# Performance work log

Measured on AMD Instinct MI355X. Metric: run time of the kernel, lower is better.

The kernel has to match this reference:

```python
import jax, jax.numpy as jnp
import numpy as np

N = 100_000      # nodes
E = 1_600_000    # edges (avg degree 16)
F_IN = 128       # dataset.num_features
H = 128          # hidden
C = 25_000       # num_clusters (~ target_ratio 0.25 * N)
G = 64           # graphs in batch
NCLS = 10        # dataset.num_classes


def _gcn_conv(x, w, b, src, dst, n):
    # PyG GCNConv: add self loops, symmetric normalization deg^-1/2 A_hat deg^-1/2
    h = x @ w  # [n, out]
    deg = jnp.zeros((n,), x.dtype).at[dst].add(1.0) + 1.0  # +1 self loop
    dis = jax.lax.rsqrt(deg)
    norm = dis[src] * dis[dst]  # [E]
    out = jnp.zeros_like(h).at[dst].add(h[src] * norm[:, None])
    out = out + h * (dis * dis)[:, None]  # self-loop term norm_ii = deg_i^-1
    return out + b


def _mean_pool(x, seg, num_seg):
    s = jax.ops.segment_sum(x, seg, num_segments=num_seg)
    cnt = jax.ops.segment_sum(jnp.ones((x.shape[0],), x.dtype), seg, num_segments=num_seg)
    return s / jnp.maximum(cnt, 1.0)[:, None]


def _max_pool(x, seg, num_seg):
    m = jax.ops.segment_max(x, seg, num_segments=num_seg)
    cnt = jax.ops.segment_sum(jnp.ones((x.shape[0],), x.dtype), seg, num_segments=num_seg)
    return jnp.where(cnt[:, None] > 0, m, 0.0)


def setup_inputs() -> dict:
    key = jax.random.key(0)
    ks = jax.random.split(key, 12)
    def glorot(k, shape):
        fan_in = shape[0]
        return (jax.random.normal(k, shape, jnp.float32) / np.sqrt(fan_in)).astype(jnp.float32)
    return {
        "x": jax.random.normal(ks[0], (N, F_IN), jnp.float32),
        "edge_index": jax.random.randint(ks[1], (2, E), 0, N, dtype=jnp.int32).astype(jnp.int64),
        "batch": jnp.sort(jax.random.randint(ks[2], (N,), 0, G, dtype=jnp.int32)).astype(jnp.int64),
        "cluster": jax.random.randint(ks[3], (N,), 0, C, dtype=jnp.int32).astype(jnp.int64),
        "num_clusters": C,
        "num_graphs": G,
        "W1": glorot(ks[4], (F_IN, H)), "b1": jnp.zeros((H,), jnp.float32),
        "W2": glorot(ks[5], (H, H)),   "b2": jnp.zeros((H,), jnp.float32),
        "W3": glorot(ks[6], (H, H)),   "b3": jnp.zeros((H,), jnp.float32),
        "lin1_w": glorot(ks[7], (4 * H, H)), "lin1_b": jnp.zeros((H,), jnp.float32),
        "lin2_w": glorot(ks[8], (H, NCLS)),  "lin2_b": jnp.zeros((NCLS,), jnp.float32),
    }


def reference(x, edge_index, batch, cluster, num_clusters, num_graphs,
              W1, b1, W2, b2, W3, b3, lin1_w, lin1_b, lin2_w, lin2_b):
    n = x.shape[0]
    src, dst = edge_index[0], edge_index[1]
    # conv1 + relu (dropout is identity in eval mode)
    h = jax.nn.relu(_gcn_conv(x, W1, b1, src, dst, n))
    pre_mean = _mean_pool(h, batch, num_graphs)
    pre_max = _max_pool(h, batch, num_graphs)
    # LaCorePooling(aggregate='mean'): segment-mean nodes by cluster id,
    # relabel edges to cluster ids, derive pooled batch vector.
    hp = _mean_pool(h, cluster, num_clusters)            # [C, H]
    src_p, dst_p = cluster[src], cluster[dst]            # pooled edge list
    batch_p = jax.ops.segment_max(batch, cluster, num_segments=num_clusters)
    batch_p = jnp.maximum(batch_p, 0)                    # empty clusters -> graph 0
    # post-pool GCN layers
    hp = jax.nn.relu(_gcn_conv(hp, W2, b2, src_p, dst_p, num_clusters))
    hp = jax.nn.relu(_gcn_conv(hp, W3, b3, src_p, dst_p, num_clusters))
    post_mean = _mean_pool(hp, batch_p, num_graphs)
    post_max = _max_pool(hp, batch_p, num_graphs)
    z = jnp.concatenate([pre_mean, pre_max, post_mean, post_max], axis=-1)  # [G, 4H]
    z = jax.nn.relu(z @ lin1_w + lin1_b)
    z = z @ lin2_w + lin2_b
    return jax.nn.log_softmax(z, axis=-1)
```

## Files before the change

### kernel.cpp

```cpp
#include <hip/hip_runtime.h>

constexpr int N_NODES = 100000;
constexpr int N_EDGES = 1600000;
constexpr int N_CLUST = 25000;
constexpr int N_GRAPH = 64;
constexpr int NCLSN   = 10;

constexpr int BKT1_SHIFT = 9;
constexpr int NBKT1 = (N_NODES + 511) / 512;
constexpr int EPB = 4096;
constexpr int NEB = (N_EDGES + EPB - 1) / EPB;
constexpr int SORT_CAP = 12288;

constexpr int SCAN_BPB = 1024;
constexpr int NB1 = (N_NODES + SCAN_BPB - 1) / SCAN_BPB;
constexpr int NB2 = (N_CLUST + SCAN_BPB - 1) / SCAN_BPB;
constexpr int NB3 = (N_CLUST + SCAN_BPB - 1) / SCAN_BPB;
constexpr int NBT = NB1 + NB2 + NB3;

__device__ __forceinline__ float bf16lo(unsigned u){ return __uint_as_float(u << 16); }
__device__ __forceinline__ float bf16hi(unsigned u){ return __uint_as_float(u & 0xffff0000u); }
__device__ __forceinline__ unsigned bf16_rne(float f){
  unsigned u = __float_as_uint(f);
  return (u + 0x7fffu + ((u >> 16) & 1u)) >> 16;
}
__device__ __forceinline__ unsigned pack2(float lo, float hi){
  return bf16_rne(lo) | (bf16_rne(hi) << 16);
}

typedef short bf16x8 __attribute__((ext_vector_type(8)));
typedef float f32x4  __attribute__((ext_vector_type(4)));

__launch_bounds__(1024)
__global__ void count_kernel(const int* __restrict__ ei, int* __restrict__ bhist){
  __shared__ int h1c[NBKT1];
  int t = threadIdx.x;
  for (int i = t; i < NBKT1; i += 1024) h1c[i] = 0;
  __syncthreads();
  int e0 = blockIdx.x * EPB;
  #pragma unroll
  for (int i = 0; i < EPB / 1024; ++i){
    int e = e0 + i * 1024 + t;
    if (e < N_EDGES) atomicAdd(&h1c[ei[N_EDGES + e] >> BKT1_SHIFT], 1);
  }
  __syncthreads();
  for (int i = t; i < NBKT1; i += 1024) bhist[blockIdx.x * NBKT1 + i] = h1c[i];
}

__launch_bounds__(512)
__global__ void colscan(const int* __restrict__ bhist, int* __restrict__ boffs,
                        int* __restrict__ gcnt1){
  __shared__ int s[512];
  int i = blockIdx.x;
  int t = threadIdx.x;
  int v = (t < NEB) ? bhist[t * NBKT1 + i] : 0;
  s[t] = v; __syncthreads();
  for (int o = 1; o < 512; o <<= 1){
    int a = (t >= o) ? s[t - o] : 0;
    __syncthreads(); s[t] += a; __syncthreads();
  }
  if (t < NEB) boffs[t * NBKT1 + i] = s[t] - v;
  if (t == 511) gcnt1[i] = s[511];
}

__launch_bounds__(256)
__global__ void bucket_scan(const int* __restrict__ gcnt1, int* __restrict__ gbase1){
  __shared__ int s[256];
  int t = threadIdx.x;
  int v = (t < NBKT1) ? gcnt1[t] : 0;
  s[t] = v; __syncthreads();
  for (int off = 1; off < 256; off <<= 1){
    int a = (t >= off) ? s[t - off] : 0;
    __syncthreads(); s[t] += a; __syncthreads();
  }
  if (t < NBKT1) gbase1[t] = s[t] - v;
}

__launch_bounds__(1024)
__global__ void scatter_kernel(const int* __restrict__ ei, const int* __restrict__ gbase1,
                               const int* __restrict__ boffs, unsigned int* __restrict__ stage1){
  __shared__ int gb1[NBKT1];
  __shared__ int cur[NBKT1];
  int t = threadIdx.x, b = blockIdx.x;
  for (int i = t; i < NBKT1; i += 1024){
    gb1[i] = gbase1[i] + boffs[b * NBKT1 + i];
    cur[i] = 0;
  }
  __syncthreads();
  int e0 = b * EPB;
  #pragma unroll
  for (int i = 0; i < EPB / 1024; ++i){
    int e = e0 + i * 1024 + t;
    if (e < N_EDGES){
      int src = ei[e], dst = ei[N_EDGES + e];
      int bk = dst >> BKT1_SHIFT;
      int r = atomicAdd(&cur[bk], 1);
      stage1[gb1[bk] + r] = ((unsigned)(dst & 511) << 17) | (unsigned)src;
    }
  }
}

__launch_bounds__(1024)
__global__ void bucket_sort(const unsigned int* __restrict__ stage, const int* __restrict__ gbase,
                            const int* __restrict__ gcnt, int* __restrict__ outpay,
                            int* __restrict__ deg){
  __shared__ int cnt[512], off[512];
  __shared__ int sorted[SORT_CAP];
  int b = blockIdx.x, t = threadIdx.x;
  int base = gbase[b], n = gcnt[b];
  if (t < 512) cnt[t] = 0;
  __syncthreads();
  for (int i = t; i < n; i += 1024) atomicAdd(&cnt[stage[base + i] >> 17], 1);
  __syncthreads();
  if (t < 512){
    int idx = b * 512 + t;
    if (idx < N_NODES) deg[idx] = cnt[t];
    off[t] = cnt[t];
  }
  __syncthreads();
  for (int s = 1; s < 512; s <<= 1){
    int v = 0;
    if (t < 512 && t >= s) v = off[t - s];
    __syncthreads();
    if (t < 512) off[t] += v;
    __syncthreads();
  }
  if (t < 512) off[t] -= cnt[t];
  __syncthreads();
  if (n <= SORT_CAP){
    for (int i = t; i < n; i += 1024){
      unsigned w = stage[base + i];
      int r = atomicAdd(&off[w >> 17], 1);
      sorted[r] = (int)(w & 0x1FFFFu);
    }
    __syncthreads();
    for (int i = t; i < n; i += 1024) outpay[base + i] = sorted[i];
  } else {
    for (int i = t; i < n; i += 1024){
      unsigned w = stage[base + i];
      int r = atomicAdd(&off[w >> 17], 1);
      outpay[base + r] = (int)(w & 0x1FFFFu);
    }
  }
}

__global__ void node_prep(const int* __restrict__ cluster, const int* __restrict__ deg1,
                          int* __restrict__ cntn, int* __restrict__ deg2){
  int v = blockIdx.x * blockDim.x + threadIdx.x;
  if (v < N_NODES){
    int c = cluster[v];
    atomicAdd(&cntn[c], 1);
    atomicAdd(&deg2[c], deg1[v]);
  }
}

__device__ __forceinline__ void seg_select(int b, const int* deg1, const int* cntn,
                                           const int* deg2, const int*& src, int& n, int& base){
  if (b < NB1){ src = deg1; n = N_NODES; base = b * SCAN_BPB; }
  else if (b < NB1 + NB2){ src = cntn; n = N_CLUST; base = (b - NB1) * SCAN_BPB; }
  else { src = deg2; n = N_CLUST; base = (b - NB1 - NB2) * SCAN_BPB; }
}

__launch_bounds__(256)
__global__ void block_sums(const int* __restrict__ deg1, const int* __restrict__ cntn,
                           const int* __restrict__ deg2, int* __restrict__ bsum){
  int b = blockIdx.x;
  const int* src; int n, base;
  seg_select(b, deg1, cntn, deg2, src, n, base);
  int t = threadIdx.x;
  int i0 = base + t * 4;
  int s = 0;
  if (i0 + 3 < n){ int4 v = *(const int4*)&src[i0]; s = v.x + v.y + v.z + v.w; }
  else { for (int j = 0; j < 4; ++j){ int i = i0 + j; if (i < n) s += src[i]; } }
  __shared__ int sh[256];
  sh[t] = s; __syncthreads();
  for (int off = 128; off > 0; off >>= 1){
    if (t < off) sh[t] += sh[t + off];
    __syncthreads();
  }
  if (t == 0) bsum[b] = sh[0];
}

__launch_bounds__(256)
__global__ void scan_bsums(const int* __restrict__ bsum, int* __restrict__ boff,
                           int* __restrict__ rowptr1, int* __restrict__ rowptrn,
                           int* __restrict__ rowptr2){
  __shared__ int s[256];
  int t = threadIdx.x;
  int v = (t < NBT) ? bsum[t] : 0;
  s[t] = v; __syncthreads();
  int seg = (t < NB1) ? 0 : (t < NB1 + NB2 ? 1 : 2);
  for (int off = 1; off < 256; off <<= 1){
    int add = 0;
    if (t >= off){
      int u = t - off;
      int useg = (u < NB1) ? 0 : (u < NB1 + NB2 ? 1 : 2);
      if (useg == seg) add = s[u];
    }
    __syncthreads();
    s[t] += add;
    __syncthreads();
  }
  if (t < NBT) boff[t] = s[t] - v;
  if (t == NB1 - 1)       rowptr1[N_NODES] = s[t];
  if (t == NB1 + NB2 - 1) rowptrn[N_CLUST] = s[t];
  if (t == NBT - 1)       rowptr2[N_CLUST] = s[t];
}

__launch_bounds__(256)
__global__ void scan_final(const int* __restrict__ deg1, const int* __restrict__ cntn,
                           const int* __restrict__ deg2, const int* __restrict__ boff,
                           int* __restrict__ rowptr1, float* __restrict__ dis1,
                           int* __restrict__ rowptrn, int* __restrict__ curn,
                           int* __restrict__ rowptr2, float* __restrict__ dis2){
  int b = blockIdx.x;
  const int* src; int n, base;
  seg_select(b, deg1, cntn, deg2, src, n, base);
  int* rp; int* cur; float* dis;
  if (b < NB1){ rp = rowptr1; cur = nullptr; dis = dis1; }
  else if (b < NB1 + NB2){ rp = rowptrn; cur = curn; dis = nullptr; }
  else { rp = rowptr2; cur = nullptr; dis = dis2; }
  int t = threadIdx.x;
  int i0 = base + t * 4;
  int v[4]; int s = 0;
  #pragma unroll
  for (int j = 0; j < 4; ++j){ int i = i0 + j; v[j] = (i < n) ? src[i] : 0; s += v[j]; }
  __shared__ int sh[256];
  sh[t] = s; __syncthreads();
  for (int off = 1; off < 256; off <<= 1){
    int add = (t >= off) ? sh[t - off] : 0;
    __syncthreads();
    sh[t] += add;
    __syncthreads();
  }
  int run = sh[t] - s + boff[b];
  #pragma unroll
  for (int j = 0; j < 4; ++j){
    int i = i0 + j;
    if (i < n){
      rp[i] = run;
      if (cur) cur[i] = run;
      if (dis) dis[i] = rsqrtf((float)v[j] + 1.0f);
      run += v[j];
    }
  }
}

__global__ void fill_n(const int* __restrict__ cluster, int* __restrict__ curn,
                       int* __restrict__ nidx){
  int v = blockIdx.x * blockDim.x + threadIdx.x;
  if (v >= N_NODES) return;
  nidx[atomicAdd(&curn[cluster[v]], 1)] = v;
}

__launch_bounds__(256)
__global__ void psrc_build(const int* __restrict__ rowptrn, const int* __restrict__ nidx,
                           const int* __restrict__ rowptr1, const int* __restrict__ esrc1,
                           const int* __restrict__ cluster, const int* __restrict__ rowptr2,
                           int* __restrict__ psrcC){
  int c = blockIdx.x * 4 + (threadIdx.x >> 6);
  int l = threadIdx.x & 63;
  int mb = rowptrn[c], me = rowptrn[c + 1];
  int cnt = me - mb;
  int base_l = 0, d_l = 0;
  if (l < cnt){
    int v = nidx[mb + l];
    base_l = rowptr1[v];
    d_l = rowptr1[v + 1] - base_l;
  }
  int pref = d_l;
  #pragma unroll
  for (int off = 1; off < 64; off <<= 1){
    int u = __shfl_up(pref, off);
    if (l >= off) pref += u;
  }
  int total = __shfl(pref, 63);
  int wbase = rowptr2[c];
  int iters = (total + 63) >> 6;
  for (int k = 0; k < iters; ++k){
    int idx = k * 64 + l;
    int idxc = min(idx, total - 1);
    int m = 0;
    for (int j = 0; j < cnt; ++j){
      int pj = __shfl(pref, j);
      if (idxc >= pj) m = j + 1;
    }
    int pm = __shfl(pref, m);
    int dm = __shfl(d_l, m);
    int bm = __shfl(base_l, m);
    int e = bm + idxc - (pm - dm);
    int sc = cluster[esrc1[e]];
    if (idx < total) psrcC[wbase + idx] = sc;
  }
}

template<bool A_BF16>
__launch_bounds__(256)
__global__ void gemm_mfma(const void* __restrict__ Aptr, const float* __restrict__ B,
                          const float* __restrict__ scale, unsigned* __restrict__ Cmat,
                          int M){
  __shared__ __align__(16) unsigned Blds[128 * 68];
  __shared__ __align__(16) unsigned Alds[64 * 68];
  const int t = threadIdx.x;
  const int row0 = blockIdx.x * 64;

  #pragma unroll
  for (int i = 0; i < 8; ++i){
    int task = t + i * 256;
    int kp = task >> 5, nq = task & 31;
    float4 b0 = *(const float4*)&B[(2 * kp) * 128 + nq * 4];
    float4 b1 = *(const float4*)&B[(2 * kp + 1) * 128 + nq * 4];
    Blds[(nq * 4 + 0) * 68 + kp] = pack2(b0.x, b1.x);
    Blds[(nq * 4 + 1) * 68 + kp] = pack2(b0.y, b1.y);
    Blds[(nq * 4 + 2) * 68 + kp] = pack2(b0.z, b1.z);
    Blds[(nq * 4 + 3) * 68 + kp] = pack2(b0.w, b1.w);
  }
  if (A_BF16){
    const unsigned* A = (const unsigned*)Aptr;
    #pragma unroll
    for (int i = 0; i < 8; ++i){
      int idx = t + i * 256;
      int row = idx >> 5, c2 = idx & 31;
      int grow = min(row0 + row, M - 1);
      uint2 v = *(const uint2*)&A[(size_t)grow * 64 + c2 * 2];
      Alds[row * 68 + c2 * 2]     = v.x;
      Alds[row * 68 + c2 * 2 + 1] = v.y;
    }
  } else {
    const float* A = (const float*)Aptr;
    #pragma unroll
    for (int i = 0; i < 8; ++i){
      int idx = t + i * 256;
      int row = idx >> 5, k4 = idx & 31;
      int grow = min(row0 + row, M - 1);
      float4 v = *(const float4*)&A[(size_t)grow * 128 + k4 * 4];
      Alds[row * 68 + k4 * 2]     = pack2(v.x, v.y);
      Alds[row * 68 + k4 * 2 + 1] = pack2(v.z, v.w);
    }
  }
  __syncthreads();

  const int wv = t >> 6, l = t & 63, quad = l >> 4, n16 = l & 15;
  f32x4 acc[8];
  #pragma unroll
  for (int nt = 0; nt < 8; ++nt) acc[nt] = (f32x4){0.f, 0.f, 0.f, 0.f};
  const int arow = wv * 16 + n16;
  #pragma unroll
  for (int ks = 0; ks < 4; ++ks){
    bf16x8 af = *(const bf16x8*)&Alds[arow * 68 + ks * 16 + quad * 4];
    #pragma unroll
    for (int nt = 0; nt < 8; ++nt){
      bf16x8 bfr = *(const bf16x8*)&Blds[(nt * 16 + n16) * 68 + ks * 16 + quad * 4];
      acc[nt] = __builtin_amdgcn_mfma_f32_16x16x32_bf16(af, bfr, acc[nt], 0, 0, 0);
    }
  }
  #pragma unroll
  for (int nt = 0; nt < 8; ++nt){
    #pragma unroll
    for (int r = 0; r < 4; ++r){
      int row = row0 + wv * 16 + quad * 4 + r;
      float sc = scale[min(row, M - 1)];
      float v = acc[nt][r] * sc;
      float vhi = __shfl_xor(v, 1);
      if (((l & 1) == 0) && row < M)
        Cmat[(size_t)row * 64 + nt * 8 + (n16 >> 1)] = pack2(v, vhi);
    }
  }
}

__launch_bounds__(256)
__global__ void conv_csr(const unsigned* __restrict__ Ts, const float* __restrict__ dis,
                         const int* __restrict__ rowptr, const int* __restrict__ esrc,
                         const float* __restrict__ bias, unsigned* __restrict__ Hout){
  int w = blockIdx.x * 4 + (threadIdx.x >> 6);
  int l = threadIdx.x & 63;
  int q = l & 15, h = l >> 4;
  int beg = rowptr[w], end = rowptr[w + 1];
  float acc[8] = {0.f,0.f,0.f,0.f,0.f,0.f,0.f,0.f};
  for (int base = beg; base < end; base += 64){
    int n = min(64, end - base);
    int eid = esrc[base + min(l, n - 1)];
    int j = 0;
    for (; j + 8 <= n; j += 8){
      int s0 = __shfl(eid, j + h);
      int s1 = __shfl(eid, j + 4 + h);
      uint4 u0 = *(const uint4*)&Ts[(size_t)s0 * 64 + q * 4];
      uint4 u1 = *(const uint4*)&Ts[(size_t)s1 * 64 + q * 4];
      acc[0] += bf16lo(u0.x); acc[1] += bf16hi(u0.x);
      acc[2] += bf16lo(u0.y); acc[3] += bf16hi(u0.y);
      acc[4] += bf16lo(u0.z); acc[5] += bf16hi(u0.z);
      acc[6] += bf16lo(u0.w); acc[7] += bf16hi(u0.w);
      acc[0] += bf16lo(u1.x); acc[1] += bf16hi(u1.x);
      acc[2] += bf16lo(u1.y); acc[3] += bf16hi(u1.y);
      acc[4] += bf16lo(u1.z); acc[5] += bf16hi(u1.z);
      acc[6] += bf16lo(u1.w); acc[7] += bf16hi(u1.w);
    }
    for (; j < n; j += 4){
      int ei = j + h;
      int s = __shfl(eid, min(ei, n - 1));
      uint4 u = *(const uint4*)&Ts[(size_t)s * 64 + q * 4];
      if (ei < n){
        acc[0] += bf16lo(u.x); acc[1] += bf16hi(u.x);
        acc[2] += bf16lo(u.y); acc[3] += bf16hi(u.y);
        acc[4] += bf16lo(u.z); acc[5] += bf16hi(u.z);
        acc[6] += bf16lo(u.w); acc[7] += bf16hi(u.w);
      }
    }
  }
  #pragma unroll
  for (int k = 0; k < 8; ++k){
    acc[k] += __shfl_xor(acc[k], 16);
    acc[k] += __shfl_xor(acc[k], 32);
  }
  float d = dis[w];
  uint4 us = *(const uint4*)&Ts[(size_t)w * 64 + q * 4];
  float4 b0 = *(const float4*)&bias[q * 8];
  float4 b1 = *(const float4*)&bias[q * 8 + 4];
  float r0 = fmaxf(fmaf(d, acc[0] + bf16lo(us.x), b0.x), 0.f);
  float r1 = fmaxf(fmaf(d, acc[1] + bf16hi(us.x), b0.y), 0.f);
  float r2 = fmaxf(fmaf(d, acc[2] + bf16lo(us.y), b0.z), 0.f);
  float r3 = fmaxf(fmaf(d, acc[3] + bf16hi(us.y), b0.w), 0.f);
  float r4 = fmaxf(fmaf(d, acc[4] + bf16lo(us.z), b1.x), 0.f);
  float r5 = fmaxf(fmaf(d, acc[5] + bf16hi(us.z), b1.y), 0.f);
  float r6 = fmaxf(fmaf(d, acc[6] + bf16lo(us.w), b1.z), 0.f);
  float r7 = fmaxf(fmaf(d, acc[7] + bf16hi(us.w), b1.w), 0.f);
  if (h == 0){
    uint4 o;
    o.x = pack2(r0, r1); o.y = pack2(r2, r3);
    o.z = pack2(r4, r5); o.w = pack2(r6, r7);
    *(uint4*)&Hout[(size_t)w * 64 + q * 4] = o;
  }
}

__launch_bounds__(256)
__global__ void cluster_gather(const unsigned* __restrict__ h1, const int* __restrict__ rowptrn,
                               const int* __restrict__ nidx, const int* __restrict__ batch,
                               unsigned* __restrict__ hp, int* __restrict__ batchp){
  int c = blockIdx.x * 4 + (threadIdx.x >> 6);
  int l = threadIdx.x & 63;
  int q = l & 15, h = l >> 4;
  int mb = rowptrn[c], me = rowptrn[c + 1];
  float acc[8] = {0.f,0.f,0.f,0.f,0.f,0.f,0.f,0.f};
  int vmax = -1;
  for (int base = mb; base < me; base += 64){
    int n = min(64, me - base);
    int vid = nidx[base + min(l, n - 1)];
    if (l < n) vmax = max(vmax, vid);
    int j = 0;
    for (; j + 8 <= n; j += 8){
      int s0 = __shfl(vid, j + h);
      int s1 = __shfl(vid, j + 4 + h);
      uint4 u0 = *(const uint4*)&h1[(size_t)s0 * 64 + q * 4];
      uint4 u1 = *(const uint4*)&h1[(size_t)s1 * 64 + q * 4];
      acc[0] += bf16lo(u0.x); acc[1] += bf16hi(u0.x);
      acc[2] += bf16lo(u0.y); acc[3] += bf16hi(u0.y);
      acc[4] += bf16lo(u0.z); acc[5] += bf16hi(u0.z);
      acc[6] += bf16lo(u0.w); acc[7] += bf16hi(u0.w);
      acc[0] += bf16lo(u1.x); acc[1] += bf16hi(u1.x);
      acc[2] += bf16lo(u1.y); acc[3] += bf16hi(u1.y);
      acc[4] += bf16lo(u1.z); acc[5] += bf16hi(u1.z);
      acc[6] += bf16lo(u1.w); acc[7] += bf16hi(u1.w);
    }
    for (; j < n; j += 4){
      int ei = j + h;
      int s = __shfl(vid, min(ei, n - 1));
      uint4 u = *(const uint4*)&h1[(size_t)s * 64 + q * 4];
      if (ei < n){
        acc[0] += bf16lo(u.x); acc[1] += bf16hi(u.x);
        acc[2] += bf16lo(u.y); acc[3] += bf16hi(u.y);
        acc[4] += bf16lo(u.z); acc[5] += bf16hi(u.z);
        acc[6] += bf16lo(u.w); acc[7] += bf16hi(u.w);
      }
    }
  }
  #pragma unroll
  for (int k = 0; k < 8; ++k){
    acc[k] += __shfl_xor(acc[k], 16);
    acc[k] += __shfl_xor(acc[k], 32);
  }
  #pragma unroll
  for (int off = 32; off > 0; off >>= 1) vmax = max(vmax, __shfl_xor(vmax, off));
  float inv = 1.0f / (float)max(me - mb, 1);
  if (h == 0){
    uint4 o;
    o.x = pack2(acc[0] * inv, acc[1] * inv);
    o.y = pack2(acc[2] * inv, acc[3] * inv);
    o.z = pack2(acc[4] * inv, acc[5] * inv);
    o.w = pack2(acc[6] * inv, acc[7] * inv);
    *(uint4*)&hp[(size_t)c * 64 + q * 4] = o;
  }
  if (l == 0) batchp[c] = (vmax >= 0) ? batch[vmax] : 0;
}

__global__ void cntp_kernel(const int* __restrict__ batchp, int* __restrict__ cntp){
  int c = blockIdx.x * blockDim.x + threadIdx.x;
  if (c < N_CLUST) atomicAdd(&cntp[batchp[c]], 1);
}

__global__ void scan_cntp(const int* __restrict__ cntp, int* __restrict__ gbasep,
                          int* __restrict__ curp){
  int t = threadIdx.x;
  int v = cntp[t];
  int s = v;
  for (int off = 1; off < 64; off <<= 1){
    int u = __shfl_up(s, off);
    if (t >= off) s += u;
  }
  gbasep[t] = s - v; curp[t] = s - v;
  if (t == 63) gbasep[64] = s;
}

__global__ void fill_c(const int* __restrict__ batchp, int* __restrict__ curp,
                       int* __restrict__ cidx){
  int c = blockIdx.x * blockDim.x + threadIdx.x;
  if (c < N_CLUST) cidx[atomicAdd(&curp[batchp[c]], 1)] = c;
}

__global__ void graph_bounds(const int* __restrict__ batch, int* __restrict__ gstart){
  int g = threadIdx.x;
  if (g > N_GRAPH) return;
  int lo = 0, hi = N_NODES;
  while (lo < hi){ int mid = (lo + hi) >> 1; if (batch[mid] < g) lo = mid + 1; else hi = mid; }
  gstart[g] = lo;
}

__device__ __forceinline__ void atomicMaxPosF(float* addr, float v){
  atomicMax((int*)addr, __float_as_int(v));
}

constexpr int PRE_SPLIT = 8;
__launch_bounds__(256)
__global__ void pre_pool_g(const unsigned* __restrict__ h1, const int* __restrict__ gstart,
                           float* __restrict__ psum, float* __restrict__ pmax){
  int g = blockIdx.x / PRE_SPLIT, sp = blockIdx.x % PRE_SPLIT;
  int t = threadIdx.x, w = t >> 6, l = t & 63;
  int s0 = gstart[g], s1 = gstart[g + 1];
  int n = s1 - s0;
  int per = (n + PRE_SPLIT - 1) / PRE_SPLIT;
  int b0 = s0 + sp * per, b1 = min(b0 + per, s1);
  float2 a0{0.f,0.f}, a1{0.f,0.f}, a2{0.f,0.f}, a3{0.f,0.f};
  float2 mx{0.f,0.f};
  int i = b0 + w;
  for (; i + 12 < b1; i += 16){
    unsigned u0 = h1[(size_t)(i     ) * 64 + l];
    unsigned u1 = h1[(size_t)(i +  4) * 64 + l];
    unsigned u2 = h1[(size_t)(i +  8) * 64 + l];
    unsigned u3 = h1[(size_t)(i + 12) * 64 + l];
    float f0x = bf16lo(u0), f0y = bf16hi(u0);
    float f1x = bf16lo(u1), f1y = bf16hi(u1);
    float f2x = bf16lo(u2), f2y = bf16hi(u2);
    float f3x = bf16lo(u3), f3y = bf16hi(u3);
    a0.x += f0x; a0.y += f0y; a1.x += f1x; a1.y += f1y;
    a2.x += f2x; a2.y += f2y; a3.x += f3x; a3.y += f3y;
    mx.x = fmaxf(fmaxf(mx.x, fmaxf(f0x, f1x)), fmaxf(f2x, f3x));
    mx.y = fmaxf(fmaxf(mx.y, fmaxf(f0y, f1y)), fmaxf(f2y, f3y));
  }
  for (; i < b1; i += 4){
    unsigned u = h1[(size_t)i * 64 + l];
    float fx = bf16lo(u), fy = bf16hi(u);
    a0.x += fx; a0.y += fy;
    mx.x = fmaxf(mx.x, fx); mx.y = fmaxf(mx.y, fy);
  }
  __shared__ float2 ssum[4][64], smax[4][64];
  ssum[w][l] = { a0.x + a1.x + a2.x + a3.x, a0.y + a1.y + a2.y + a3.y };
  smax[w][l] = mx;
  __syncthreads();
  if (w == 0){
    float2 S = ssum[0][l], M = smax[0][l];
    #pragma unroll
    for (int k = 1; k < 4; ++k){
      S.x += ssum[k][l].x; S.y += ssum[k][l].y;
      M.x = fmaxf(M.x, smax[k][l].x); M.y = fmaxf(M.y, smax[k][l].y);
    }
    atomicAdd(&psum[g * 128 + 2 * l], S.x);
    atomicAdd(&psum[g * 128 + 2 * l + 1], S.y);
    atomicMaxPosF(&pmax[g * 128 + 2 * l], M.x);
    atomicMaxPosF(&pmax[g * 128 + 2 * l + 1], M.y);
  }
}

constexpr int POST_SPLIT = 4;
__launch_bounds__(256)
__global__ void post_pool_g(const unsigned* __restrict__ hp3, const int* __restrict__ gbasep,
                            const int* __restrict__ cidx,
                            float* __restrict__ psum, float* __restrict__ pmax){
  int g = blockIdx.x / POST_SPLIT, sp = blockIdx.x % POST_SPLIT;
  int t = threadIdx.x, w = t >> 6, l = t & 63;
  int s0 = gbasep[g], s1 = gbasep[g + 1];
  int n = s1 - s0;
  int per = (n + POST_SPLIT * 4 - 1) / (POST_SPLIT * 4);
  int b0 = s0 + (sp * 4 + w) * per, b1 = min(b0 + per, s1);
  float2 a0{0.f,0.f}, a1{0.f,0.f}, a2{0.f,0.f}, a3{0.f,0.f};
  float2 mx{0.f,0.f};
  for (int base = b0; base < b1; base += 64){
    int nn = min(64, b1 - base);
    int cid = cidx[base + min(l, nn - 1)];
    int j = 0;
    for (; j + 4 <= nn; j += 4){
      int c0 = __shfl(cid, j);
      int c1 = __shfl(cid, j + 1);
      int c2 = __shfl(cid, j + 2);
      int c3 = __shfl(cid, j + 3);
      unsigned u0 = hp3[(size_t)c0 * 64 + l];
      unsigned u1 = hp3[(size_t)c1 * 64 + l];
      unsigned u2 = hp3[(size_t)c2 * 64 + l];
      unsigned u3 = hp3[(size_t)c3 * 64 + l];
      float f0x = bf16lo(u0), f0y = bf16hi(u0);
      float f1x = bf16lo(u1), f1y = bf16hi(u1);
      float f2x = bf16lo(u2), f2y = bf16hi(u2);
      float f3x = bf16lo(u3), f3y = bf16hi(u3);
      a0.x += f0x; a0.y += f0y; a1.x += f1x; a1.y += f1y;
      a2.x += f2x; a2.y += f2y; a3.x += f3x; a3.y += f3y;
      mx.x = fmaxf(fmaxf(mx.x, fmaxf(f0x, f1x)), fmaxf(f2x, f3x));
      mx.y = fmaxf(fmaxf(mx.y, fmaxf(f0y, f1y)), fmaxf(f2y, f3y));
    }
    for (; j < nn; ++j){
      int c = __shfl(cid, j);
      unsigned u = hp3[(size_t)c * 64 + l];
      float fx = bf16lo(u), fy = bf16hi(u);
      a0.x += fx; a0.y += fy;
      mx.x = fmaxf(mx.x, fx); mx.y = fmaxf(mx.y, fy);
    }
  }
  __shared__ float2 ssum[4][64], smax[4][64];
  ssum[w][l] = { a0.x + a1.x + a2.x + a3.x, a0.y + a1.y + a2.y + a3.y };
  smax[w][l] = mx;
  __syncthreads();
  if (w == 0){
    float2 S = ssum[0][l], M = smax[0][l];
    #pragma unroll
    for (int k = 1; k < 4; ++k){
      S.x += ssum[k][l].x; S.y += ssum[k][l].y;
      M.x = fmaxf(M.x, smax[k][l].x); M.y = fmaxf(M.y, smax[k][l].y);
    }
    atomicAdd(&psum[g * 128 + 2 * l], S.x);
    atomicAdd(&psum[g * 128 + 2 * l + 1], S.y);
    atomicMaxPosF(&pmax[g * 128 + 2 * l], M.x);
    atomicMaxPosF(&pmax[g * 128 + 2 * l + 1], M.y);
  }
}

__launch_bounds__(128)
__global__ void head_kernel(const float* __restrict__ psum, const float* __restrict__ pmax,
                            const float* __restrict__ postsum, const float* __restrict__ postmax,
                            const int* __restrict__ gstart, const int* __restrict__ cntp,
                            const float* __restrict__ l1w, const float* __restrict__ l1b,
                            const float* __restrict__ l2w, const float* __restrict__ l2b,
                            float* __restrict__ out){
  int g = blockIdx.x, t = threadIdx.x;
  __shared__ float z[512];
  __shared__ float a[128];
  __shared__ float logits[16];
  __shared__ float lse_s;
  float cpre  = (float)max(gstart[g + 1] - gstart[g], 1);
  float cpost = fmaxf((float)cntp[g], 1.0f);
  z[t]       = psum[g * 128 + t] / cpre;
  z[128 + t] = pmax[g * 128 + t];
  z[256 + t] = postsum[g * 128 + t] / cpost;
  z[384 + t] = postmax[g * 128 + t];
  __syncthreads();
  float acc = l1b[t];
  #pragma unroll 8
  for (int k = 0; k < 512; ++k) acc = fmaf(z[k], l1w[k * 128 + t], acc);
  a[t] = fmaxf(acc, 0.f);
  __syncthreads();
  if (t < NCLSN){
    float s2 = l2b[t];
    for (int k = 0; k < 128; ++k) s2 = fmaf(a[k], l2w[k * NCLSN + t], s2);
    logits[t] = s2;
  }
  __syncthreads();
  if (t == 0){
    float m = logits[0];
    for (int c = 1; c < NCLSN; ++c) m = fmaxf(m, logits[c]);
    float s = 0.f;
    for (int c = 0; c < NCLSN; ++c) s += expf(logits[c] - m);
    lse_s = m + logf(s);
  }
  __syncthreads();
  if (t < NCLSN) out[g * NCLSN + t] = logits[t] - lse_s;
}

extern "C" void kernel_launch(void* const* d_in, const int* in_sizes, int n_in,
                              void* d_out, int out_size, void* d_ws, size_t ws_size,
                              hipStream_t stream){
  const float* x       = (const float*)d_in[0];
  const int*   ei      = (const int*)  d_in[1];
  const int*   batch   = (const int*)  d_in[2];
  const int*   cluster = (const int*)  d_in[3];
  const float* W1      = (const float*)d_in[6];
  const float* b1      = (const float*)d_in[7];
  const float* W2      = (const float*)d_in[8];
  const float* b2      = (const float*)d_in[9];
  const float* W3      = (const float*)d_in[10];
  const float* b3      = (const float*)d_in[11];
  const float* l1w     = (const float*)d_in[12];
  const float* l1b     = (const float*)d_in[13];
  const float* l2w     = (const float*)d_in[14];
  const float* l2b     = (const float*)d_in[15];
  float* out = (float*)d_out;

  char* base = (char*)d_ws;
  size_t off = 0;
  auto alloc = [&](size_t bytes) -> char* {
    char* p = base + off;
    off += (bytes + 255) & ~size_t(255);
    return p;
  };
  char*  zbase  = base + off;
  int*   cntn   = (int*)  alloc((size_t)N_CLUST * 4);
  int*   deg2   = (int*)  alloc((size_t)N_CLUST * 4);
  int*   cntp   = (int*)  alloc((size_t)N_GRAPH * 4);
  float* pre_s  = (float*)alloc((size_t)N_GRAPH * 128 * 4);
  float* pre_m  = (float*)alloc((size_t)N_GRAPH * 128 * 4);
  float* post_s = (float*)alloc((size_t)N_GRAPH * 128 * 4);
  float* post_m = (float*)alloc((size_t)N_GRAPH * 128 * 4);
  size_t zsize = off;
  unsigned* Ts1   = (unsigned*)alloc((size_t)N_NODES * 64 * 4);
  unsigned* h1    = (unsigned*)alloc((size_t)N_NODES * 64 * 4);
  int*   esrc1   = (int*)  alloc((size_t)N_EDGES * 4);
  int*   psrcC   = (int*)  alloc((size_t)N_EDGES * 4);
  int*   deg1    = (int*)  alloc((size_t)N_NODES * 4);
  int*   rowptr1 = (int*)  alloc((size_t)(N_NODES + 1) * 4);
  int*   rowptrn = (int*)  alloc((size_t)(N_CLUST + 1) * 4);
  int*   curn    = (int*)  alloc((size_t)N_CLUST * 4);
  int*   rowptr2 = (int*)  alloc((size_t)(N_CLUST + 1) * 4);
  int*   nidx    = (int*)  alloc((size_t)N_NODES * 4);
  float* dis1    = (float*)alloc((size_t)N_NODES * 4);
  float* dis2    = (float*)alloc((size_t)N_CLUST * 4);
  int*   batchp  = (int*)  alloc((size_t)N_CLUST * 4);
  int*   gstart  = (int*)  alloc((size_t)(N_GRAPH + 1) * 4);
  int*   bsum    = (int*)  alloc((size_t)NBT * 4);
  int*   boff    = (int*)  alloc((size_t)NBT * 4);
  int*   gcnt1   = (int*)  alloc((size_t)NBKT1 * 4);
  int*   gbase1  = (int*)  alloc((size_t)NBKT1 * 4);
  int*   bhist   = (int*)  alloc((size_t)NEB * NBKT1 * 4);
  int*   boffs   = (int*)  alloc((size_t)NEB * NBKT1 * 4);
  int*   gbasep  = (int*)  alloc((size_t)(N_GRAPH + 1) * 4);
  int*   curp    = (int*)  alloc((size_t)N_GRAPH * 4);
  int*   cidx    = (int*)  alloc((size_t)N_CLUST * 4);
  unsigned int* stage1 = (unsigned int*)h1;
  unsigned* hp  = Ts1;
  unsigned* Ts2 = Ts1 + (size_t)N_CLUST * 64;
  unsigned* hp2 = Ts1 + (size_t)2 * N_CLUST * 64;
  unsigned* hp3 = Ts1 + (size_t)3 * N_CLUST * 64;
  unsigned* Ts3 = Ts2;

  (void)in_sizes; (void)n_in; (void)out_size; (void)ws_size;

  hipMemsetAsync(zbase, 0, zsize, stream);

  count_kernel  <<<NEB, 1024, 0, stream>>>(ei, bhist);
  colscan       <<<NBKT1, 512, 0, stream>>>(bhist, boffs, gcnt1);
  bucket_scan   <<<1, 256, 0, stream>>>(gcnt1, gbase1);
  scatter_kernel<<<NEB, 1024, 0, stream>>>(ei, gbase1, boffs, stage1);
  bucket_sort   <<<NBKT1, 1024, 0, stream>>>(stage1, gbase1, gcnt1, esrc1, deg1);
  node_prep<<<(N_NODES + 255) / 256, 256, 0, stream>>>(cluster, deg1, cntn, deg2);
  block_sums <<<NBT, 256, 0, stream>>>(deg1, cntn, deg2, bsum);
  scan_bsums <<<1, 256, 0, stream>>>(bsum, boff, rowptr1, rowptrn, rowptr2);
  scan_final <<<NBT, 256, 0, stream>>>(deg1, cntn, deg2, boff,
                                       rowptr1, dis1, rowptrn, curn, rowptr2, dis2);
  fill_n<<<(N_NODES + 255) / 256, 256, 0, stream>>>(cluster, curn, nidx);
  psrc_build<<<N_CLUST / 4, 256, 0, stream>>>(rowptrn, nidx, rowptr1, esrc1,
                                              cluster, rowptr2, psrcC);

  gemm_mfma<false><<<(N_NODES + 63) / 64, 256, 0, stream>>>(x, W1, dis1, Ts1, N_NODES);
  conv_csr<<<N_NODES / 4, 256, 0, stream>>>(Ts1, dis1, rowptr1, esrc1, b1, h1);

  graph_bounds<<<1, 128, 0, stream>>>(batch, gstart);
  pre_pool_g<<<N_GRAPH * PRE_SPLIT, 256, 0, stream>>>(h1, gstart, pre_s, pre_m);

  cluster_gather<<<N_CLUST / 4, 256, 0, stream>>>(h1, rowptrn, nidx, batch, hp, batchp);
  cntp_kernel<<<(N_CLUST + 255) / 256, 256, 0, stream>>>(batchp, cntp);
  scan_cntp<<<1, 64, 0, stream>>>(cntp, gbasep, curp);
  fill_c<<<(N_CLUST + 255) / 256, 256, 0, stream>>>(batchp, curp, cidx);

  gemm_mfma<true><<<(N_CLUST + 63) / 64, 256, 0, stream>>>(hp, W2, dis2, Ts2, N_CLUST);
  conv_csr<<<N_CLUST / 4, 256, 0, stream>>>(Ts2, dis2, rowptr2, psrcC, b2, hp2);

  gemm_mfma<true><<<(N_CLUST + 63) / 64, 256, 0, stream>>>(hp2, W3, dis2, Ts3, N_CLUST);
  conv_csr<<<N_CLUST / 4, 256, 0, stream>>>(Ts3, dis2, rowptr2, psrcC, b3, hp3);

  post_pool_g<<<N_GRAPH * POST_SPLIT, 256, 0, stream>>>(hp3, gbasep, cidx, post_s, post_m);
  head_kernel<<<N_GRAPH, 128, 0, stream>>>(pre_s, pre_m, post_s, post_m, gstart, cntp,
                                           l1w, l1b, l2w, l2b, out);
}
```

Measured before the change: 546.0 us.

## Replace CSR gather-sum aggregation with MFMA one-hot scatter over 16-row groups

Each wave now handles 16 destination rows. Their incoming edges plus self-loops are gathered in chunks of 32 into LDS. A one-hot selection matrix built from the destination bits packed into the edge payload then lets an MFMA do the summation. The packing widens the stored payload mask to carry destination-within-group bits, and psrc_build tags pooled edges the same way. This trades scalar FP adds and per-row wave underutilisation for extra LDS traffic, shuffles and mostly-zero MFMA work. High-degree groups also process many chunks serially.

```diff
diff --git a/kernel.cpp b/kernel.cpp
--- a/kernel.cpp
+++ b/kernel.cpp
@@ -11,6 +11,8 @@
 constexpr int EPB = 4096;
 constexpr int NEB = (N_EDGES + EPB - 1) / EPB;
 constexpr int SORT_CAP = 12288;
+
+constexpr unsigned PAY_SRC_MASK = 0x1FFFFu;
 
 constexpr int SCAN_BPB = 1024;
 constexpr int NB1 = (N_NODES + SCAN_BPB - 1) / SCAN_BPB;
@@ -131,7 +133,7 @@
     for (int i = t; i < n; i += 1024){
       unsigned w = stage[base + i];
       int r = atomicAdd(&off[w >> 17], 1);
-      sorted[r] = (int)(w & 0x1FFFFu);
+      sorted[r] = (int)(w & 0x1FFFFFu);
     }
     __syncthreads();
     for (int i = t; i < n; i += 1024) outpay[base + i] = sorted[i];
@@ -139,7 +141,7 @@
     for (int i = t; i < n; i += 1024){
       unsigned w = stage[base + i];
       int r = atomicAdd(&off[w >> 17], 1);
-      outpay[base + r] = (int)(w & 0x1FFFFu);
+      outpay[base + r] = (int)(w & 0x1FFFFFu);
     }
   }
 }
@@ -276,6 +278,7 @@
   }
   int total = __shfl(pref, 63);
   int wbase = rowptr2[c];
+  int dbits = (c & 15) << 17;
   int iters = (total + 63) >> 6;
   for (int k = 0; k < iters; ++k){
     int idx = k * 64 + l;
@@ -289,8 +292,8 @@
     int dm = __shfl(d_l, m);
     int bm = __shfl(base_l, m);
     int e = bm + idxc - (pm - dm);
-    int sc = cluster[esrc1[e]];
-    if (idx < total) psrcC[wbase + idx] = sc;
+    int sc = cluster[esrc1[e] & (int)PAY_SRC_MASK];
+    if (idx < total) psrcC[wbase + idx] = sc | dbits;
   }
 }
 
@@ -368,67 +371,89 @@
   }
 }
 
-__launch_bounds__(256)
-__global__ void conv_csr(const unsigned* __restrict__ Ts, const float* __restrict__ dis,
-                         const int* __restrict__ rowptr, const int* __restrict__ esrc,
-                         const float* __restrict__ bias, unsigned* __restrict__ Hout){
-  int w = blockIdx.x * 4 + (threadIdx.x >> 6);
-  int l = threadIdx.x & 63;
-  int q = l & 15, h = l >> 4;
-  int beg = rowptr[w], end = rowptr[w + 1];
-  float acc[8] = {0.f,0.f,0.f,0.f,0.f,0.f,0.f,0.f};
-  for (int base = beg; base < end; base += 64){
-    int n = min(64, end - base);
-    int eid = esrc[base + min(l, n - 1)];
-    int j = 0;
-    for (; j + 8 <= n; j += 8){
-      int s0 = __shfl(eid, j + h);
-      int s1 = __shfl(eid, j + 4 + h);
-      uint4 u0 = *(const uint4*)&Ts[(size_t)s0 * 64 + q * 4];
-      uint4 u1 = *(const uint4*)&Ts[(size_t)s1 * 64 + q * 4];
-      acc[0] += bf16lo(u0.x); acc[1] += bf16hi(u0.x);
-      acc[2] += bf16lo(u0.y); acc[3] += bf16hi(u0.y);
-      acc[4] += bf16lo(u0.z); acc[5] += bf16hi(u0.z);
-      acc[6] += bf16lo(u0.w); acc[7] += bf16hi(u0.w);
-      acc[0] += bf16lo(u1.x); acc[1] += bf16hi(u1.x);
-      acc[2] += bf16lo(u1.y); acc[3] += bf16hi(u1.y);
-      acc[4] += bf16lo(u1.z); acc[5] += bf16hi(u1.z);
-      acc[6] += bf16lo(u1.w); acc[7] += bf16hi(u1.w);
-    }
-    for (; j < n; j += 4){
-      int ei = j + h;
-      int s = __shfl(eid, min(ei, n - 1));
-      uint4 u = *(const uint4*)&Ts[(size_t)s * 64 + q * 4];
-      if (ei < n){
-        acc[0] += bf16lo(u.x); acc[1] += bf16hi(u.x);
-        acc[2] += bf16lo(u.y); acc[3] += bf16hi(u.y);
-        acc[4] += bf16lo(u.z); acc[5] += bf16hi(u.z);
-        acc[6] += bf16lo(u.w); acc[7] += bf16hi(u.w);
-      }
-    }
-  }
-  #pragma unroll
-  for (int k = 0; k < 8; ++k){
-    acc[k] += __shfl_xor(acc[k], 16);
-    acc[k] += __shfl_xor(acc[k], 32);
-  }
-  float d = dis[w];
-  uint4 us = *(const uint4*)&Ts[(size_t)w * 64 + q * 4];
-  float4 b0 = *(const float4*)&bias[q * 8];
-  float4 b1 = *(const float4*)&bias[q * 8 + 4];
-  float r0 = fmaxf(fmaf(d, acc[0] + bf16lo(us.x), b0.x), 0.f);
-  float r1 = fmaxf(fmaf(d, acc[1] + bf16hi(us.x), b0.y), 0.f);
-  float r2 = fmaxf(fmaf(d, acc[2] + bf16lo(us.y), b0.z), 0.f);
-  float r3 = fmaxf(fmaf(d, acc[3] + bf16hi(us.y), b0.w), 0.f);
-  float r4 = fmaxf(fmaf(d, acc[4] + bf16lo(us.z), b1.x), 0.f);
-  float r5 = fmaxf(fmaf(d, acc[5] + bf16hi(us.z), b1.y), 0.f);
-  float r6 = fmaxf(fmaf(d, acc[6] + bf16lo(us.w), b1.z), 0.f);
-  float r7 = fmaxf(fmaf(d, acc[7] + bf16hi(us.w), b1.w), 0.f);
-  if (h == 0){
-    uint4 o;
-    o.x = pack2(r0, r1); o.y = pack2(r2, r3);
-    o.z = pack2(r4, r5); o.w = pack2(r6, r7);
-    *(uint4*)&Hout[(size_t)w * 64 + q * 4] = o;
+constexpr int BSTR = 17;
+
+__launch_bounds__(256, 4)
+__global__ void conv_mfma(const unsigned* __restrict__ Ts, const float* __restrict__ dis,
+                          const int* __restrict__ rowptr, const int* __restrict__ epay,
+                          const float* __restrict__ bias, unsigned* __restrict__ Hout,
+                          int M){
+  __shared__ unsigned Blds[4][128 * BSTR];
+  const int t = threadIdx.x, wv = t >> 6, l = t & 63;
+  const int gi = blockIdx.x * 4 + wv;
+  const int base = gi * 16;
+  if (base >= M) return;
+  const int n16 = l & 15, quad = l >> 4;
+  const int beg = rowptr[base];
+  const int end = rowptr[min(base + 16, M)];
+  const int cnt = end - beg;
+  const int selfN = min(16, M - base);
+  const int total = cnt + selfN;
+  const int nch = (total + 31) >> 5;
+  unsigned* Bl = &Blds[wv][0];
+
+  f32x4 acc[8];
+  #pragma unroll
+  for (int nt = 0; nt < 8; ++nt) acc[nt] = (f32x4){0.f, 0.f, 0.f, 0.f};
+  float bv[8];
+  #pragma unroll
+  for (int nt = 0; nt < 8; ++nt) bv[nt] = bias[nt * 16 + n16];
+
+  for (int ch = 0; ch < nch; ++ch){
+    int ke = ch * 32 + (l & 31);
+    int d, src;
+    if (ke < cnt){
+      int p = epay[beg + ke];
+      src = p & (int)PAY_SRC_MASK;
+      d = (p >> 17) & 15;
+    } else {
+      int sd = ke - cnt;
+      d   = (sd < selfN) ? sd : 31;
+      src = (sd < selfN) ? (base + sd) : 0;
+    }
+    #pragma unroll
+    for (int i = 0; i < 4; ++i){
+      int pp = quad + i * 4;
+      int s0 = __shfl(src, 2 * pp);
+      int s1 = __shfl(src, 2 * pp + 1);
+      uint4 u0 = *(const uint4*)&Ts[(size_t)s0 * 64 + n16 * 4];
+      uint4 u1 = *(const uint4*)&Ts[(size_t)s1 * 64 + n16 * 4];
+      unsigned* wp = Bl + (n16 * 8) * BSTR + pp;
+      wp[0 * BSTR] = __builtin_amdgcn_perm(u1.x, u0.x, 0x05040100u);
+      wp[1 * BSTR] = __builtin_amdgcn_perm(u1.x, u0.x, 0x07060302u);
+      wp[2 * BSTR] = __builtin_amdgcn_perm(u1.y, u0.y, 0x05040100u);
+      wp[3 * BSTR] = __builtin_amdgcn_perm(u1.y, u0.y, 0x07060302u);
+      wp[4 * BSTR] = __builtin_amdgcn_perm(u1.z, u0.z, 0x05040100u);
+      wp[5 * BSTR] = __builtin_amdgcn_perm(u1.z, u0.z, 0x07060302u);
+      wp[6 * BSTR] = __builtin_amdgcn_perm(u1.w, u0.w, 0x05040100u);
+      wp[7 * BSTR] = __builtin_amdgcn_perm(u1.w, u0.w, 0x07060302u);
+    }
+    union { unsigned u[4]; bf16x8 v; } af;
+    #pragma unroll
+    for (int jj = 0; jj < 4; ++jj){
+      int d0 = __shfl(d, quad * 8 + 2 * jj);
+      int d1 = __shfl(d, quad * 8 + 2 * jj + 1);
+      af.u[jj] = (d0 == n16 ? 0x3F80u : 0u) | (d1 == n16 ? 0x3F800000u : 0u);
+    }
+    #pragma unroll
+    for (int nt = 0; nt < 8; ++nt){
+      union { unsigned u[4]; bf16x8 v; } bf;
+      const unsigned* rp = Bl + (nt * 16 + n16) * BSTR + quad * 4;
+      bf.u[0] = rp[0]; bf.u[1] = rp[1]; bf.u[2] = rp[2]; bf.u[3] = rp[3];
+      acc[nt] = __builtin_amdgcn_mfma_f32_16x16x32_bf16(af.v, bf.v, acc[nt], 0, 0, 0);
+    }
+  }
+  #pragma unroll
+  for (int r = 0; r < 4; ++r){
+    int row = base + quad * 4 + r;
+    float dsc = dis[min(row, M - 1)];
+    #pragma unroll
+    for (int nt = 0; nt < 8; ++nt){
+      float v = fmaxf(fmaf(dsc, acc[nt][r], bv[nt]), 0.f);
+      float vhi = __shfl_xor(v, 1);
+      if (((l & 1) == 0) && row < M)
+        Hout[(size_t)row * 64 + nt * 8 + (n16 >> 1)] = pack2(v, vhi);
+    }
   }
 }
 
@@ -764,8 +789,10 @@
   psrc_build<<<N_CLUST / 4, 256, 0, stream>>>(rowptrn, nidx, rowptr1, esrc1,
                                               cluster, rowptr2, psrcC);
 
+  constexpr int NG1 = N_NODES / 16;
+  constexpr int NG2 = (N_CLUST + 15) / 16;
   gemm_mfma<false><<<(N_NODES + 63) / 64, 256, 0, stream>>>(x, W1, dis1, Ts1, N_NODES);
-  conv_csr<<<N_NODES / 4, 256, 0, stream>>>(Ts1, dis1, rowptr1, esrc1, b1, h1);
+  conv_mfma<<<(NG1 + 3) / 4, 256, 0, stream>>>(Ts1, dis1, rowptr1, esrc1, b1, h1, N_NODES);
 
   graph_bounds<<<1, 128, 0, stream>>>(batch, gstart);
   pre_pool_g<<<N_GRAPH * PRE_SPLIT, 256, 0, stream>>>(h1, gstart, pre_s, pre_m);
@@ -776,10 +803,10 @@
   fill_c<<<(N_CLUST + 255) / 256, 256, 0, stream>>>(batchp, curp, cidx);
 
   gemm_mfma<true><<<(N_CLUST + 63) / 64, 256, 0, stream>>>(hp, W2, dis2, Ts2, N_CLUST);
-  conv_csr<<<N_CLUST / 4, 256, 0, stream>>>(Ts2, dis2, rowptr2, psrcC, b2, hp2);
+  conv_mfma<<<(NG2 + 3) / 4, 256, 0, stream>>>(Ts2, dis2, rowptr2, psrcC, b2, hp2, N_CLUST);
 
   gemm_mfma<true><<<(N_CLUST + 63) / 64, 256, 0, stream>>>(hp2, W3, dis2, Ts3, N_CLUST);
-  conv_csr<<<N_CLUST / 4, 256, 0, stream>>>(Ts3, dis2, rowptr2, psrcC, b3, hp3);
+  conv_mfma<<<(NG2 + 3) / 4, 256, 0, stream>>>(Ts3, dis2, rowptr2, psrcC, b3, hp3, N_CLUST);
 
   post_pool_g<<<N_GRAPH * POST_SPLIT, 256, 0, stream>>>(hp3, gbasep, cidx, post_s, post_m);
   head_kernel<<<N_GRAPH, 128, 0, stream>>>(pre_s, pre_m, post_s, post_m, gstart, cntp,
```

After: 628.4 us. 15.1% more time.

## Pack destination low bits into sorted edge payload and unroll CSR gather to 16

Applied to the files above, without the earlier changes.

The bucket sort now keeps four extra bits of the staged word (destination low bits) in the payload, and the pooled edge build tags each cluster source with the destination's low four bits. Consumers mask the payload back to the 17-bit source index. The CSR aggregation adds a 16-edge unrolled step so four 16-byte row loads are in flight at once, aiming to hide gather latency. The extra bits are not yet used anywhere, and the added masking and unroll raise register use.

```diff
diff --git a/kernel.cpp b/kernel.cpp
--- a/kernel.cpp
+++ b/kernel.cpp
@@ -11,6 +11,8 @@
 constexpr int EPB = 4096;
 constexpr int NEB = (N_EDGES + EPB - 1) / EPB;
 constexpr int SORT_CAP = 12288;
+
+constexpr unsigned PAY_SRC_MASK = 0x1FFFFu;
 
 constexpr int SCAN_BPB = 1024;
 constexpr int NB1 = (N_NODES + SCAN_BPB - 1) / SCAN_BPB;
@@ -131,7 +133,7 @@
     for (int i = t; i < n; i += 1024){
       unsigned w = stage[base + i];
       int r = atomicAdd(&off[w >> 17], 1);
-      sorted[r] = (int)(w & 0x1FFFFu);
+      sorted[r] = (int)(w & 0x1FFFFFu);
     }
     __syncthreads();
     for (int i = t; i < n; i += 1024) outpay[base + i] = sorted[i];
@@ -139,7 +141,7 @@
     for (int i = t; i < n; i += 1024){
       unsigned w = stage[base + i];
       int r = atomicAdd(&off[w >> 17], 1);
-      outpay[base + r] = (int)(w & 0x1FFFFu);
+      outpay[base + r] = (int)(w & 0x1FFFFFu);
     }
   }
 }
@@ -276,6 +278,7 @@
   }
   int total = __shfl(pref, 63);
   int wbase = rowptr2[c];
+  int dbits = (c & 15) << 17;
   int iters = (total + 63) >> 6;
   for (int k = 0; k < iters; ++k){
     int idx = k * 64 + l;
@@ -289,8 +292,8 @@
     int dm = __shfl(d_l, m);
     int bm = __shfl(base_l, m);
     int e = bm + idxc - (pm - dm);
-    int sc = cluster[esrc1[e]];
-    if (idx < total) psrcC[wbase + idx] = sc;
+    int sc = cluster[esrc1[e] & (int)PAY_SRC_MASK];
+    if (idx < total) psrcC[wbase + idx] = sc | dbits;
   }
 }
 
@@ -379,8 +382,34 @@
   float acc[8] = {0.f,0.f,0.f,0.f,0.f,0.f,0.f,0.f};
   for (int base = beg; base < end; base += 64){
     int n = min(64, end - base);
-    int eid = esrc[base + min(l, n - 1)];
+    int eid = esrc[base + min(l, n - 1)] & (int)PAY_SRC_MASK;
     int j = 0;
+    for (; j + 16 <= n; j += 16){
+      int s0 = __shfl(eid, j + h);
+      int s1 = __shfl(eid, j + 4 + h);
+      int s2 = __shfl(eid, j + 8 + h);
+      int s3 = __shfl(eid, j + 12 + h);
+      uint4 u0 = *(const uint4*)&Ts[(size_t)s0 * 64 + q * 4];
+      uint4 u1 = *(const uint4*)&Ts[(size_t)s1 * 64 + q * 4];
+      uint4 u2 = *(const uint4*)&Ts[(size_t)s2 * 64 + q * 4];
+      uint4 u3 = *(const uint4*)&Ts[(size_t)s3 * 64 + q * 4];
+      acc[0] += bf16lo(u0.x); acc[1] += bf16hi(u0.x);
+      acc[2] += bf16lo(u0.y); acc[3] += bf16hi(u0.y);
+      acc[4] += bf16lo(u0.z); acc[5] += bf16hi(u0.z);
+      acc[6] += bf16lo(u0.w); acc[7] += bf16hi(u0.w);
+      acc[0] += bf16lo(u1.x); acc[1] += bf16hi(u1.x);
+      acc[2] += bf16lo(u1.y); acc[3] += bf16hi(u1.y);
+      acc[4] += bf16lo(u1.z); acc[5] += bf16hi(u1.z);
+      acc[6] += bf16lo(u1.w); acc[7] += bf16hi(u1.w);
+      acc[0] += bf16lo(u2.x); acc[1] += bf16hi(u2.x);
+      acc[2] += bf16lo(u2.y); acc[3] += bf16hi(u2.y);
+      acc[4] += bf16lo(u2.z); acc[5] += bf16hi(u2.z);
+      acc[6] += bf16lo(u2.w); acc[7] += bf16hi(u2.w);
+      acc[0] += bf16lo(u3.x); acc[1] += bf16hi(u3.x);
+      acc[2] += bf16lo(u3.y); acc[3] += bf16hi(u3.y);
+      acc[4] += bf16lo(u3.z); acc[5] += bf16hi(u3.z);
+      acc[6] += bf16lo(u3.w); acc[7] += bf16hi(u3.w);
+    }
     for (; j + 8 <= n; j += 8){
       int s0 = __shfl(eid, j + h);
       int s1 = __shfl(eid, j + 4 + h);
```

Result: no change. 538.3 us (-1.4%).
